# Optimization experiments

Hardware: AMD Instinct MI355X
Metric: run time of the kernel (lower is better)

## Reference

```python
import jax, jax.numpy as jnp
import numpy as np

H, B, N, D, VD, FFH = 8, 16, 512, 512, 64, 2048
NPICK = N // 2
NORM = 1.0 / np.sqrt(VD)


def _ha_encoder(h, W_query, W_key, W_val, W1, W2, W3, W4, W5, W6):
    # h: [B, N, D]; weights: [H, D, VD]
    np_ = NPICK
    pick, dlv = h[:, :np_], h[:, np_:]
    proj = lambda x, W: jnp.einsum('bnd,hdk->hbnk', x, W)
    Q, K, V = proj(h, W_query), proj(h, W_key), proj(h, W_val)
    Kp, Kd = K[:, :, :np_], K[:, :, np_:]   # shared projections (same W_key)
    Vp, Vd = V[:, :, :np_], V[:, :, np_:]
    Qp = proj(pick, W1); Qpap = proj(pick, W2); Qpad = proj(pick, W3)
    Qd = proj(dlv, W4);  Qdad = proj(dlv, W5);  Qdap = proj(dlv, W6)
    c_main = NORM * jnp.einsum('hbnk,hbmk->hbnm', Q, K)          # [H,B,N,N]
    c_pd = NORM * jnp.sum(Qp * Kd, -1)                           # [H,B,np] paired pick->delivery
    c_pap = NORM * jnp.einsum('hbnk,hbmk->hbnm', Qpap, Kp)       # pick -> all pick
    c_pad = NORM * jnp.einsum('hbnk,hbmk->hbnm', Qpad, Kd)       # pick -> all delivery
    c_dp = NORM * jnp.sum(Qd * Kp, -1)                           # paired delivery->pick
    c_dad = NORM * jnp.einsum('hbnk,hbmk->hbnm', Qdad, Kd)       # delivery -> all delivery
    c_dap = NORM * jnp.einsum('hbnk,hbmk->hbnm', Qdap, Kp)       # delivery -> all pick
    ninf1 = jnp.full((H, h.shape[0], np_), -jnp.inf, c_main.dtype)
    ninf2 = jnp.full((H, h.shape[0], np_, np_), -jnp.inf, c_main.dtype)
    col_pd = jnp.concatenate([c_pd, ninf1], 2)[..., None]        # [H,B,N,1]
    blk_pap = jnp.concatenate([c_pap, ninf2], 2)                 # [H,B,N,np]
    blk_pad = jnp.concatenate([c_pad, ninf2], 2)
    col_dp = jnp.concatenate([ninf1, c_dp], 2)[..., None]
    blk_dad = jnp.concatenate([ninf2, c_dad], 2)
    blk_dap = jnp.concatenate([ninf2, c_dap], 2)
    compat = jnp.concatenate([c_main, col_pd, blk_pap, blk_pad, col_dp, blk_dad, blk_dap], -1)
    a = jax.nn.softmax(compat, -1)                               # [H,B,N,N+2+4*np]
    zpad = jnp.zeros_like(Vd)
    V_add_d = jnp.concatenate([Vd, zpad], 2)                     # [H,B,N,VD]
    V_add_p = jnp.concatenate([zpad, Vp], 2)
    av = lambda w, v: jnp.einsum('hbnm,hbmv->hbnv', w, v)
    i = N
    heads = av(a[..., :N], V)
    heads = heads + a[..., i:i + 1] * V_add_d; i += 1
    heads = heads + av(a[..., i:i + np_], Vp); i += np_
    heads = heads + av(a[..., i:i + np_], Vd); i += np_
    heads = heads + a[..., i:i + 1] * V_add_p; i += 1
    heads = heads + av(a[..., i:i + np_], Vd); i += np_
    heads = heads + av(a[..., i:i + np_], Vp)
    return heads.transpose(1, 2, 0, 3).reshape(h.shape[0], N, H * VD)


def _split_heads(x):
    b, n, hd = x.shape
    return x.reshape(b, n, H, hd // H).transpose(0, 2, 1, 3)


def _mha(q, k, v):
    dk = q.shape[-1]
    w = jax.nn.softmax(jnp.einsum('bhnd,bhmd->bhnm', q, k) / np.sqrt(dk), -1)
    o = jnp.einsum('bhnm,bhmd->bhnd', w, v)
    b, hh, n, d = o.shape
    return o.transpose(0, 2, 1, 3).reshape(b, n, hh * d)


def _ff(x, w1, b1, w2, b2, a):
    return x + (jax.nn.relu(x @ w1 + b1) @ w2 + b2) * a


def _forward(x, W_query, W_key, W_val, W1_query, W2_query, W3_query, W4_query, W5_query, W6_query,
             Wq_w, Wk_w, Wv_w, Wq2p_w, Wq2d_w, Wk2_w, Wv2_w,
             comb_w, comb_b, comb2_w, comb2_b, comb3_w, comb3_b,
             alpha1, alpha2, alpha3,
             ff1_w1, ff1_b1, ff1_w2, ff1_b2, ffa1,
             ff2_w1, ff2_b1, ff2_w2, ff2_b2, ffa2,
             ff3_w1, ff3_b1, ff3_w2, ff3_b2, ffa3):
    # stage 1: heterogeneous attention block (combine_3 / AN3 / FF3)
    ha = _ha_encoder(x, W_query, W_key, W_val, W1_query, W2_query, W3_query, W4_query, W5_query, W6_query)
    out = x + (ha @ comb3_w + comb3_b) * alpha3
    out = _ff(out, ff3_w1, ff3_b1, ff3_w2, ff3_b2, ffa3)
    # stage 2: standard multi-head self-attention (combine / AN1 / FF1)
    q = _split_heads(out @ Wq_w); k = _split_heads(out @ Wk_w); v = _split_heads(out @ Wv_w)
    out = out + (_mha(q, k, v) @ comb_w + comb_b) * alpha1
    out = _ff(out, ff1_w1, ff1_b1, ff1_w2, ff1_b2, ffa1)
    # stage 3: pickup/delivery specific queries (combine_2 / AN2 / FF2)
    q2 = jnp.concatenate([out[:, :NPICK] @ Wq2p_w, out[:, NPICK:] @ Wq2d_w], 1)
    q2 = _split_heads(q2); k2 = _split_heads(out @ Wk2_w); v2 = _split_heads(out @ Wv2_w)
    out = out + (_mha(q2, k2, v2) @ comb2_w + comb2_b) * alpha2
    out = _ff(out, ff2_w1, ff2_b1, ff2_w2, ff2_b2, ffa2)
    return out


def setup_inputs() -> dict:
    key = jax.random.key(0)
    ks = jax.random.split(key, 64)
    it = iter(range(64))
    def nrm(shape):
        return jax.random.normal(ks[next(it)], shape, jnp.float32)
    def uni(shape):
        s = 1.0 / np.sqrt(shape[-1])  # torch init_parameters: uniform(-1/sqrt(size(-1)), ...)
        return jax.random.uniform(ks[next(it)], shape, jnp.float32, -s, s)
    d = {'x': nrm((B, N, D))}
    for n in ['W_query', 'W_key', 'W_val', 'W1_query', 'W2_query', 'W3_query', 'W4_query', 'W5_query', 'W6_query']:
        d[n] = uni((H, D, VD))
    for n in ['Wq_w', 'Wk_w', 'Wv_w', 'Wq2p_w', 'Wq2d_w', 'Wk2_w', 'Wv2_w']:
        d[n] = uni((D, H * VD))
    for n in ['comb_w', 'comb2_w', 'comb3_w']:
        d[n] = uni((H * VD, D))
    for n in ['comb_b', 'comb2_b', 'comb3_b']:
        d[n] = uni((D,))
    for n in ['alpha1', 'alpha2', 'alpha3']:
        d[n] = uni((1,))
    for i in ['1', '2', '3']:
        d['ff' + i + '_w1'] = uni((D, FFH))
        d['ff' + i + '_b1'] = uni((FFH,))
        d['ff' + i + '_w2'] = uni((FFH, D))
        d['ff' + i + '_b2'] = uni((D,))
        d['ffa' + i] = uni((1,))
    return d


def reference(x, W_query, W_key, W_val, W1_query, W2_query, W3_query, W4_query, W5_query, W6_query,
              Wq_w, Wk_w, Wv_w, Wq2p_w, Wq2d_w, Wk2_w, Wv2_w,
              comb_w, comb_b, comb2_w, comb2_b, comb3_w, comb3_b,
              alpha1, alpha2, alpha3,
              ff1_w1, ff1_b1, ff1_w2, ff1_b2, ffa1,
              ff2_w1, ff2_b1, ff2_w2, ff2_b2, ffa2,
              ff3_w1, ff3_b1, ff3_w2, ff3_b2, ffa3):
    return _forward(x, W_query, W_key, W_val, W1_query, W2_query, W3_query, W4_query, W5_query, W6_query,
                    Wq_w, Wk_w, Wv_w, Wq2p_w, Wq2d_w, Wk2_w, Wv2_w,
                    comb_w, comb_b, comb2_w, comb2_b, comb3_w, comb3_b,
                    alpha1, alpha2, alpha3,
                    ff1_w1, ff1_b1, ff1_w2, ff1_b2, ffa1,
                    ff2_w1, ff2_b1, ff2_w2, ff2_b2, ffa2,
                    ff3_w1, ff3_b1, ff3_w2, ff3_b2, ffa3)
```

## Files before the change

kernel.cpp:

```cpp
#include <hip/hip_runtime.h>
#include <math.h>

#define Hh 8
#define Bb 16
#define Nn 512
#define Dd 512
#define VDd 64
#define NPICKk 256
#define NORMF 0.125f
#define SCL2 0.1803368801f

typedef unsigned short ushortT;
typedef __bf16 bf16x8 __attribute__((ext_vector_type(8)));
typedef float f32x4 __attribute__((ext_vector_type(4)));

struct PtrsB { const ushortT* p[12]; };
struct PtrsD { ushortT* p[6]; };
struct Ptrs9 { const float* p[9]; };
struct Ptrs10 { const float* p[10]; };
struct Ptrs6 { const float* p[6]; };

__device__ inline ushortT f2bf(float f) {
    __bf16 h = (__bf16)f;
    union { __bf16 h; ushortT u; } v; v.h = h;
    return v.u;
}
__device__ inline float bf2f(ushortT u) {
    union { unsigned int u; float f; } v; v.u = ((unsigned int)u) << 16;
    return v.f;
}
__device__ inline float exp2fast(float x) {
#if __has_builtin(__builtin_amdgcn_exp2f)
    return __builtin_amdgcn_exp2f(x);
#else
    return exp2f(x);
#endif
}
__device__ inline void gload16(const void* gptr, void* ldsptr) {
    auto g = reinterpret_cast<const __attribute__((address_space(1))) unsigned int*>(
        reinterpret_cast<uintptr_t>(gptr));
    auto l = reinterpret_cast<__attribute__((address_space(3))) unsigned int*>(
        reinterpret_cast<uintptr_t>(ldsptr));
    __builtin_amdgcn_global_load_lds(g, l, 16, 0, 0);
}

#define LIX(r, g) (((r) << 6) + ((((g) ^ ((r) & 7))) << 3))

__global__ __launch_bounds__(256) void castx(const float* __restrict__ in,
                                             ushortT* __restrict__ out) {
    int i = blockIdx.x * 256 + threadIdx.x;
    float4 v = *(const float4*)&in[(size_t)i * 4];
    ushort4 o; o.x = f2bf(v.x); o.y = f2bf(v.y); o.z = f2bf(v.z); o.w = f2bf(v.w);
    *(ushort4*)&out[(size_t)i * 4] = o;
}

__device__ inline void tbody(const float* __restrict__ in, ushortT* __restrict__ out,
                             int in_ld, int out_ld, int r0, int c0) {
    __shared__ float T[64][65];
    int tr = threadIdx.x >> 4, tc4 = (threadIdx.x & 15) * 4;
#pragma unroll
    for (int p = 0; p < 4; ++p) {
        float4 v = *(const float4*)&in[(size_t)(r0 + tr + p * 16) * in_ld + c0 + tc4];
        T[tr + p * 16][tc4 + 0] = v.x; T[tr + p * 16][tc4 + 1] = v.y;
        T[tr + p * 16][tc4 + 2] = v.z; T[tr + p * 16][tc4 + 3] = v.w;
    }
    __syncthreads();
#pragma unroll
    for (int p = 0; p < 4; ++p) {
        int orow = c0 + tr + p * 16;
        int ocol = r0 + tc4;
        ushort4 o;
        o.x = f2bf(T[tc4 + 0][tr + p * 16]);
        o.y = f2bf(T[tc4 + 1][tr + p * 16]);
        o.z = f2bf(T[tc4 + 2][tr + p * 16]);
        o.w = f2bf(T[tc4 + 3][tr + p * 16]);
        *(ushort4*)&out[(size_t)orow * out_ld + ocol] = o;
    }
}

__global__ __launch_bounds__(256) void thead(Ptrs9 s, ushortT* __restrict__ dst) {
    int w = blockIdx.z >> 3, h = blockIdx.z & 7;
    tbody(s.p[w] + (size_t)h * 512 * 64,
          dst + (size_t)w * 262144 + (size_t)h * 64 * 512,
          64, 512, blockIdx.y * 64, 0);
}
__global__ __launch_bounds__(256) void tsq(Ptrs10 s, ushortT* __restrict__ dst) {
    tbody(s.p[blockIdx.z], dst + (size_t)blockIdx.z * 262144,
          512, 512, blockIdx.y * 64, blockIdx.x * 64);
}
__global__ __launch_bounds__(256) void tff(Ptrs6 s, ushortT* __restrict__ dst) {
    int z = blockIdx.z;
    if (z < 3) { if (blockIdx.y >= 8 || blockIdx.x >= 32) return; }
    else       { if (blockIdx.y >= 32 || blockIdx.x >= 8) return; }
    int in_ld = (z < 3) ? 2048 : 512;
    int out_ld = (z < 3) ? 512 : 2048;
    tbody(s.p[z], dst + (size_t)z * 1048576, in_ld, out_ld,
          blockIdx.y * 64, blockIdx.x * 64);
}

__global__ __launch_bounds__(256) void gemm_bf(
    PtrsB Bp, PtrsD Db, const ushortT* __restrict__ A, float* __restrict__ outF,
    int M, int N, int K, const float* __restrict__ bias,
    const float* __restrict__ res, const float* __restrict__ alpha,
    int do_relu, int nroute, int vtmask, int scmask)
{
    __shared__ __align__(16) ushortT As[128 * 64];
    __shared__ __align__(16) ushortT Bs[128 * 64];
    const int tid = threadIdx.x;
    const int wid = tid >> 6, lane = tid & 63;
    const int wm = wid >> 1, wn = wid & 1;
    const int l15 = lane & 15, l4 = lane >> 4;

    int bid = blockIdx.y * gridDim.x + blockIdx.x;
    int nwg = gridDim.x * gridDim.y;
    int q = nwg >> 3;
    int swz = (bid & 7) * q + (bid >> 3);
    int bx = swz % gridDim.x, by = swz / gridDim.x;

    const int r0 = by * 128, c0 = bx * 128;
    const int half = ((r0 & (Nn - 1)) >= NPICKk) ? 1 : 0;
    const ushortT* Bt = Bp.p[((c0 >> 9) << 1) | half];
    const int cB = nroute ? (c0 & 511) : c0;

    const ushortT* aSrc[4];
    const ushortT* bSrc[4];
    char* ldsA[4];
    char* ldsB[4];
#pragma unroll
    for (int i = 0; i < 4; ++i) {
        int off = wid * 4096 + i * 1024 + lane * 16;
        int row = off >> 7;
        int sg = ((off >> 4) & 7) ^ (row & 7);
        aSrc[i] = A + (size_t)(r0 + row) * K + sg * 8;
        bSrc[i] = Bt + (size_t)(cB + row) * K + sg * 8;
        ldsA[i] = (char*)As + off;
        ldsB[i] = (char*)Bs + off;
    }

    f32x4 acc[4][4] = {};

    for (int kt = 0; kt < K; kt += 64) {
        __syncthreads();
#pragma unroll
        for (int i = 0; i < 4; ++i) {
            gload16(aSrc[i] + kt, ldsA[i]);
            gload16(bSrc[i] + kt, ldsB[i]);
        }
        asm volatile("s_waitcnt vmcnt(0)" ::: "memory");
        __syncthreads();
#pragma unroll
        for (int kk = 0; kk < 2; ++kk) {
            int g0 = kk * 4 + l4;
            bf16x8 af[4], bfv[4];
#pragma unroll
            for (int mi = 0; mi < 4; ++mi)
                af[mi] = *(const bf16x8*)&As[LIX(wm * 64 + mi * 16 + l15, g0)];
#pragma unroll
            for (int ni = 0; ni < 4; ++ni)
                bfv[ni] = *(const bf16x8*)&Bs[LIX(wn * 64 + ni * 16 + l15, g0)];
#pragma unroll
            for (int mi = 0; mi < 4; ++mi)
#pragma unroll
                for (int ni = 0; ni < 4; ++ni)
                    acc[mi][ni] = __builtin_amdgcn_mfma_f32_16x16x32_bf16(
                        bfv[ni], af[mi], acc[mi][ni], 0, 0, 0);
        }
    }

    if (nroute) {
#pragma unroll
        for (int mi = 0; mi < 4; ++mi) {
            int row = r0 + wm * 64 + mi * 16 + l15;
#pragma unroll
            for (int ni = 0; ni < 4; ++ni) {
                int col = c0 + wn * 64 + ni * 16 + l4 * 4;
                int range = col >> 9, cc = col & 511;
                ushortT* d = Db.p[range];
                f32x4 a = acc[mi][ni];
                if ((scmask >> range) & 1) {
                    a[0] *= SCL2; a[1] *= SCL2; a[2] *= SCL2; a[3] *= SCL2;
                }
                if ((vtmask >> range) & 1) {
                    size_t vb = ((size_t)(row >> 9) * Hh + (cc >> 6)) * 64 + (cc & 63);
                    int tok = row & 511;
#pragma unroll
                    for (int r = 0; r < 4; ++r)
                        d[((vb + r) << 9) + tok] = f2bf(a[r]);
                } else {
                    ushort4 o;
                    o.x = f2bf(a[0]); o.y = f2bf(a[1]);
                    o.z = f2bf(a[2]); o.w = f2bf(a[3]);
                    *(ushort4*)&d[((size_t)row << 9) + cc] = o;
                }
            }
        }
    } else {
        const float alp = alpha ? alpha[0] : 1.0f;
        ushortT* outB = Db.p[0];
#pragma unroll
        for (int mi = 0; mi < 4; ++mi) {
            int row = r0 + wm * 64 + mi * 16 + l15;
#pragma unroll
            for (int ni = 0; ni < 4; ++ni) {
                int colb = c0 + wn * 64 + ni * 16 + l4 * 4;
                f32x4 a = acc[mi][ni];
                if (bias) {
                    float4 b4 = *(const float4*)&bias[colb];
                    a[0] += b4.x; a[1] += b4.y; a[2] += b4.z; a[3] += b4.w;
                }
                if (do_relu) {
#pragma unroll
                    for (int r = 0; r < 4; ++r) a[r] = fmaxf(a[r], 0.f);
                }
#pragma unroll
                for (int r = 0; r < 4; ++r) a[r] *= alp;
                size_t idx = (size_t)row * N + colb;
                if (res) {
                    float4 r4 = *(const float4*)&res[idx];
                    a[0] += r4.x; a[1] += r4.y; a[2] += r4.z; a[3] += r4.w;
                }
                if (outF)
                    *(float4*)&outF[idx] = make_float4(a[0], a[1], a[2], a[3]);
                if (outB) {
                    ushort4 o;
                    o.x = f2bf(a[0]); o.y = f2bf(a[1]);
                    o.z = f2bf(a[2]); o.w = f2bf(a[3]);
                    *(ushort4*)&outB[idx] = o;
                }
            }
        }
    }
}

__global__ __launch_bounds__(256) void gemm64(
    const ushortT* __restrict__ Bw, const ushortT* __restrict__ A,
    float* __restrict__ outF, ushortT* __restrict__ outB,
    int M, int N, int K, const float* __restrict__ bias,
    const float* __restrict__ resf, const ushortT* __restrict__ resb,
    const float* __restrict__ alpha, int do_relu)
{
    __shared__ __align__(16) ushortT As[64 * 64];
    __shared__ __align__(16) ushortT Bs[128 * 64];
    const int tid = threadIdx.x;
    const int wid = tid >> 6, lane = tid & 63;
    const int wm = wid >> 1, wn = wid & 1;
    const int l15 = lane & 15, l4 = lane >> 4;

    int bid = blockIdx.y * gridDim.x + blockIdx.x;
    int nwg = gridDim.x * gridDim.y;
    int q = nwg >> 3;
    int swz = (bid & 7) * q + (bid >> 3);
    int bx = swz % gridDim.x, by = swz / gridDim.x;
    const int r0 = by * 64, c0 = bx * 128;

    const ushortT* aSrc[2];
    char* ldsA[2];
#pragma unroll
    for (int i = 0; i < 2; ++i) {
        int off = wid * 2048 + i * 1024 + lane * 16;
        int row = off >> 7;
        int sg = ((off >> 4) & 7) ^ (row & 7);
        aSrc[i] = A + (size_t)(r0 + row) * K + sg * 8;
        ldsA[i] = (char*)As + off;
    }
    const ushortT* bSrc[4];
    char* ldsB[4];
#pragma unroll
    for (int i = 0; i < 4; ++i) {
        int off = wid * 4096 + i * 1024 + lane * 16;
        int row = off >> 7;
        int sg = ((off >> 4) & 7) ^ (row & 7);
        bSrc[i] = Bw + (size_t)(c0 + row) * K + sg * 8;
        ldsB[i] = (char*)Bs + off;
    }

    f32x4 acc[2][4] = {};

    for (int kt = 0; kt < K; kt += 64) {
        __syncthreads();
#pragma unroll
        for (int i = 0; i < 2; ++i) gload16(aSrc[i] + kt, ldsA[i]);
#pragma unroll
        for (int i = 0; i < 4; ++i) gload16(bSrc[i] + kt, ldsB[i]);
        asm volatile("s_waitcnt vmcnt(0)" ::: "memory");
        __syncthreads();
#pragma unroll
        for (int kk = 0; kk < 2; ++kk) {
            int g0 = kk * 4 + l4;
            bf16x8 af[2], bfv[4];
#pragma unroll
            for (int mi = 0; mi < 2; ++mi)
                af[mi] = *(const bf16x8*)&As[LIX(wm * 32 + mi * 16 + l15, g0)];
#pragma unroll
            for (int ni = 0; ni < 4; ++ni)
                bfv[ni] = *(const bf16x8*)&Bs[LIX(wn * 64 + ni * 16 + l15, g0)];
#pragma unroll
            for (int mi = 0; mi < 2; ++mi)
#pragma unroll
                for (int ni = 0; ni < 4; ++ni)
                    acc[mi][ni] = __builtin_amdgcn_mfma_f32_16x16x32_bf16(
                        bfv[ni], af[mi], acc[mi][ni], 0, 0, 0);
        }
    }

    const float alp = alpha ? alpha[0] : 1.0f;
#pragma unroll
    for (int mi = 0; mi < 2; ++mi) {
        int row = r0 + wm * 32 + mi * 16 + l15;
#pragma unroll
        for (int ni = 0; ni < 4; ++ni) {
            int colb = c0 + wn * 64 + ni * 16 + l4 * 4;
            f32x4 a = acc[mi][ni];
            if (bias) {
                float4 b4 = *(const float4*)&bias[colb];
                a[0] += b4.x; a[1] += b4.y; a[2] += b4.z; a[3] += b4.w;
            }
            if (do_relu) {
#pragma unroll
                for (int r = 0; r < 4; ++r) a[r] = fmaxf(a[r], 0.f);
            }
#pragma unroll
            for (int r = 0; r < 4; ++r) a[r] *= alp;
            size_t idx = (size_t)row * N + colb;
            if (resf) {
                float4 r4 = *(const float4*)&resf[idx];
                a[0] += r4.x; a[1] += r4.y; a[2] += r4.z; a[3] += r4.w;
            }
            if (resb) {
                ushort4 r4 = *(const ushort4*)&resb[idx];
                a[0] += bf2f(r4.x); a[1] += bf2f(r4.y);
                a[2] += bf2f(r4.z); a[3] += bf2f(r4.w);
            }
            if (outF)
                *(float4*)&outF[idx] = make_float4(a[0], a[1], a[2], a[3]);
            if (outB) {
                ushort4 o;
                o.x = f2bf(a[0]); o.y = f2bf(a[1]);
                o.z = f2bf(a[2]); o.w = f2bf(a[3]);
                *(ushort4*)&outB[idx] = o;
            }
        }
    }
}

__global__ __launch_bounds__(256) void diag_dot_bb(const ushortT* __restrict__ QD,
                                                   const ushortT* __restrict__ K,
                                                   float* __restrict__ Sdg) {
    int i = blockIdx.x * 256 + threadIdx.x;
    int h = i & 7, n = (i >> 3) & 511, b = i >> 12;
    int dix = (n < NPICKk) ? n + NPICKk : n - NPICKk;
    const ushortT* q = QD + (((size_t)(b * Nn + n) * Hh + h) << 6);
    const ushortT* k = K + (((size_t)(b * Nn + dix) * Hh + h) << 6);
    float s = 0.f;
#pragma unroll
    for (int d = 0; d < 64; d += 4) {
        ushort4 a = *(const ushort4*)(q + d);
        ushort4 c = *(const ushort4*)(k + d);
        s += bf2f(a.x) * bf2f(c.x) + bf2f(a.y) * bf2f(c.y)
           + bf2f(a.z) * bf2f(c.z) + bf2f(a.w) * bf2f(c.w);
    }
    Sdg[i] = s;
}

template <int HA>
__global__ __launch_bounds__(256) void attn10(
    const ushortT* __restrict__ Qm, const ushortT* __restrict__ Km,
    const ushortT* __restrict__ Vtm, const ushortT* __restrict__ QAm,
    const ushortT* __restrict__ QBm, const float* __restrict__ Sdg,
    ushortT* __restrict__ Out)
{
    __shared__ __align__(16) ushortT Ks[64 * 64];
    __shared__ __align__(16) ushortT Vs[64 * 64];
    __shared__ __align__(16) ushortT Pw[4][16 * 64];
    __shared__ float sdl[64];

    const int tid = threadIdx.x, wid = tid >> 6, lane = tid & 63;
    const int l15 = lane & 15, l4 = lane >> 4;

    const int p = blockIdx.x + (blockIdx.y << 3) + (blockIdx.z << 6);
    const int n0 = (((p >> 3) & 7)) << 6;
    const int g8 = (p & 7) | ((p >> 6) << 3);
    const int h = g8 & 7, b = g8 >> 3;
    const int bh = b * Hh + h;

    const size_t qrow = (((size_t)(b * Nn + n0 + wid * 16 + l15) * Hh + h) << 6);
    bf16x8 qf[2], xaf[2], xbf[2];
#pragma unroll
    for (int kk = 0; kk < 2; ++kk) {
        int g0 = kk * 4 + l4;
        qf[kk] = *(const bf16x8*)&Qm[qrow + g0 * 8];
        if (HA) {
            xaf[kk] = *(const bf16x8*)&QAm[qrow + g0 * 8];
            xbf[kk] = *(const bf16x8*)&QBm[qrow + g0 * 8];
        }
    }
    if (HA && tid < 64) sdl[tid] = Sdg[((size_t)(b * Nn + n0 + tid)) * Hh + h];
    const int td = (n0 < NPICKk) ? ((n0 + NPICKk) >> 6) : ((n0 - NPICKk) >> 6);

    const ushortT* kSrc[2]; ushortT* kDst[2];
    const ushortT* vSrc[2]; ushortT* vDst[2];
#pragma unroll
    for (int i = 0; i < 2; ++i) {
        int off = wid * 2048 + i * 1024 + lane * 16;
        int row = off >> 7, sg = ((off >> 4) & 7) ^ (row & 7);
        kSrc[i] = Km + (((size_t)(b * Nn + row) * Hh + h) << 6) + sg * 8;
        kDst[i] = (ushortT*)((char*)Ks + off);
        vSrc[i] = Vtm + (((size_t)(bh * 64 + row)) << 9) + sg * 8;
        vDst[i] = (ushortT*)((char*)Vs + off);
    }

    float M[4], Lp[4];
    f32x4 Oa[4] = {};
#pragma unroll
    for (int r = 0; r < 4; ++r) { M[r] = -INFINITY; Lp[r] = 0.f; }

    bf16x8 krbuf[2][2], vrbuf[2][2];
#pragma unroll
    for (int i = 0; i < 2; ++i) {
        krbuf[0][i] = *(const bf16x8*)kSrc[i];
        vrbuf[0][i] = *(const bf16x8*)vSrc[i];
    }

#pragma unroll
    for (int t = 0; t < 8; ++t) {
        const int cur = t & 1, nxt = cur ^ 1;
        __builtin_amdgcn_s_barrier();
#pragma unroll
        for (int i = 0; i < 2; ++i) {
            *(bf16x8*)kDst[i] = krbuf[cur][i];
            *(bf16x8*)vDst[i] = vrbuf[cur][i];
        }
        if (t < 7) {
#pragma unroll
            for (int i = 0; i < 2; ++i) {
                krbuf[nxt][i] = *(const bf16x8*)(kSrc[i] + (size_t)(t + 1) * (64 * Hh * VDd));
                vrbuf[nxt][i] = *(const bf16x8*)(vSrc[i] + (t + 1) * 64);
            }
        }
        asm volatile("s_waitcnt lgkmcnt(0)" ::: "memory");
        __builtin_amdgcn_s_barrier();
        __builtin_amdgcn_sched_barrier(0);

        __builtin_amdgcn_s_setprio(1);
        f32x4 s1[4] = {}, sX[4] = {};
#pragma unroll
        for (int kk = 0; kk < 2; ++kk) {
            bf16x8 aq = qf[kk];
            bf16x8 ax;
            if (HA) ax = (t >= 4) ? xbf[kk] : xaf[kk];
#pragma unroll
            for (int ni = 0; ni < 4; ++ni) {
                bf16x8 bk = *(const bf16x8*)&Ks[LIX(ni * 16 + l15, kk * 4 + l4)];
                s1[ni] = __builtin_amdgcn_mfma_f32_16x16x32_bf16(aq, bk, s1[ni], 0, 0, 0);
                if (HA)
                    sX[ni] = __builtin_amdgcn_mfma_f32_16x16x32_bf16(ax, bk, sX[ni], 0, 0, 0);
            }
        }
        __builtin_amdgcn_s_setprio(0);

        const bool dt = HA && (t == td);

        float mloc[4];
        bool grow = false;
#pragma unroll
        for (int r = 0; r < 4; ++r) {
            int rw = wid * 16 + l4 * 4 + r;
            float m = s1[0][r];
#pragma unroll
            for (int ni = 1; ni < 4; ++ni) m = fmaxf(m, s1[ni][r]);
            if (HA) {
#pragma unroll
                for (int ni = 0; ni < 4; ++ni) m = fmaxf(m, sX[ni][r]);
            }
            if (dt && l15 == l4 * 4 + r) m = fmaxf(m, sdl[rw]);
            mloc[r] = m;
            grow = grow || (m > M[r] + 8.f);
        }
        if (__any(grow)) {
#pragma unroll
            for (int r = 0; r < 4; ++r) {
                float m = mloc[r];
#pragma unroll
                for (int o = 8; o >= 1; o >>= 1) m = fmaxf(m, __shfl_xor(m, o, 16));
                float mn = fmaxf(M[r], m);
                float sc = exp2fast(M[r] - mn);
                M[r] = mn; Lp[r] *= sc;
#pragma unroll
                for (int ni = 0; ni < 4; ++ni) Oa[ni][r] *= sc;
            }
        }

#pragma unroll
        for (int r = 0; r < 4; ++r) {
            int rw = wid * 16 + l4 * 4 + r;
            float rs = 0.f;
#pragma unroll
            for (int ni = 0; ni < 4; ++ni) {
                float pv = exp2fast(s1[ni][r] - M[r]);
                if (HA) pv += exp2fast(sX[ni][r] - M[r]);
                if (dt && ni == wid && l15 == l4 * 4 + r) pv += exp2fast(sdl[rw] - M[r]);
                s1[ni][r] = pv;
                rs += pv;
            }
            Lp[r] += rs;
        }

#pragma unroll
        for (int ni = 0; ni < 4; ++ni)
#pragma unroll
            for (int r = 0; r < 4; ++r) {
                int prow = l4 * 4 + r;
                int col = ni * 16 + l15;
                Pw[wid][(prow << 6) + ((((col >> 3) ^ (prow & 7))) << 3) + (col & 7)] =
                    f2bf(s1[ni][r]);
            }

        __builtin_amdgcn_s_setprio(1);
#pragma unroll
        for (int kk = 0; kk < 2; ++kk) {
            int g0 = kk * 4 + l4;
            bf16x8 ap = *(const bf16x8*)&Pw[wid][LIX(l15, g0)];
#pragma unroll
            for (int ni = 0; ni < 4; ++ni) {
                bf16x8 bv = *(const bf16x8*)&Vs[LIX(ni * 16 + l15, g0)];
                Oa[ni] = __builtin_amdgcn_mfma_f32_16x16x32_bf16(ap, bv, Oa[ni], 0, 0, 0);
            }
        }
        __builtin_amdgcn_s_setprio(0);
    }

#pragma unroll
    for (int r = 0; r < 4; ++r) {
        float l = Lp[r];
#pragma unroll
        for (int o = 8; o >= 1; o >>= 1) l += __shfl_xor(l, o, 16);
        float inv = 1.0f / l;
        size_t obase = (((size_t)(b * Nn + n0 + wid * 16 + l4 * 4 + r) * Hh + h) << 6);
#pragma unroll
        for (int ni = 0; ni < 4; ++ni)
            Out[obase + ni * 16 + l15] = f2bf(Oa[ni][r] * inv);
    }
}

extern "C" void kernel_launch(void* const* d_in, const int* in_sizes, int n_in,
                              void* d_out, int out_size, void* d_ws, size_t ws_size,
                              hipStream_t stream)
{
    const float* x = (const float*)d_in[0];

    int dictOrder = (in_sizes[18] != 512);
    const float* comb_w  = (const float*)d_in[17];
    const float* comb2_w = (const float*)d_in[dictOrder ? 18 : 19];
    const float* comb3_w = (const float*)d_in[dictOrder ? 19 : 21];
    const float* comb_b  = (const float*)d_in[dictOrder ? 20 : 18];
    const float* comb2_b = (const float*)d_in[dictOrder ? 21 : 20];
    const float* comb3_b = (const float*)d_in[22];
    const float* alpha1 = (const float*)d_in[23];
    const float* alpha2 = (const float*)d_in[24];
    const float* alpha3 = (const float*)d_in[25];
    const float* ff1_w1 = (const float*)d_in[26];
    const float* ff1_b1 = (const float*)d_in[27];
    const float* ff1_w2 = (const float*)d_in[28];
    const float* ff1_b2 = (const float*)d_in[29];
    const float* ffa1   = (const float*)d_in[30];
    const float* ff2_w1 = (const float*)d_in[31];
    const float* ff2_b1 = (const float*)d_in[32];
    const float* ff2_w2 = (const float*)d_in[33];
    const float* ff2_b2 = (const float*)d_in[34];
    const float* ffa2   = (const float*)d_in[35];
    const float* ff3_w1 = (const float*)d_in[36];
    const float* ff3_b1 = (const float*)d_in[37];
    const float* ff3_w2 = (const float*)d_in[38];
    const float* ff3_b2 = (const float*)d_in[39];
    const float* ffa3   = (const float*)d_in[40];

    char* W = (char*)d_ws;
    ushortT* wbHead = (ushortT*)(W + 0);
    ushortT* wbMha  = (ushortT*)(W + 4718592);
    ushortT* wbComb = (ushortT*)(W + 8388608);
    ushortT* wbFf1  = (ushortT*)(W + 9961472);
    ushortT* wbFf2  = (ushortT*)(W + 16252928);
    ushortT* xbf    = (ushortT*)(W + 22544384);
    float*   Sd     = (float*)  (W + 30932992);
    ushortT* bufQ   = (ushortT*)(W + 31195136);
    ushortT* bufK   = (ushortT*)(W + 39583744);
    ushortT* bufVt  = (ushortT*)(W + 47972352);
    ushortT* bufQA  = (ushortT*)(W + 56360960);
    ushortT* bufQB  = (ushortT*)(W + 64749568);
    ushortT* bufQD  = (ushortT*)(W + 73138176);
    ushortT* hidden = (ushortT*)(W + 81526784);
    ushortT* curb   = (ushortT*)(W + 115081216);
    ushortT* bufHA  = xbf;
    float*   cur    = (float*)d_out;

    dim3 tb(256);
    const int TOK = Bb * Nn;
    const size_t WS = 512 * 512;
    const size_t WF = 2048 * 512;

    hipLaunchKernelGGL(castx, dim3(TOK * 512 / 1024), tb, 0, stream, x, xbf);
    {
        Ptrs9 s; for (int i = 0; i < 9; ++i) s.p[i] = (const float*)d_in[1 + i];
        hipLaunchKernelGGL(thead, dim3(1, 8, 72), tb, 0, stream, s, wbHead);
    }
    {
        Ptrs10 s;
        for (int i = 0; i < 7; ++i) s.p[i] = (const float*)d_in[10 + i];
        s.p[7] = comb_w; s.p[8] = comb2_w; s.p[9] = comb3_w;
        hipLaunchKernelGGL(tsq, dim3(8, 8, 10), tb, 0, stream, s, wbMha);
    }
    {
        Ptrs6 s;
        s.p[0] = ff1_w1; s.p[1] = ff2_w1; s.p[2] = ff3_w1;
        s.p[3] = ff1_w2; s.p[4] = ff2_w2; s.p[5] = ff3_w2;
        hipLaunchKernelGGL(tff, dim3(32, 32, 6), tb, 0, stream, s, wbFf1);
    }

    auto gemm = [&](PtrsB Bp, PtrsD Db, const ushortT* A, float* oF,
                    int M, int Ncc, int Kc, const float* bias, const float* res,
                    const float* alp, int relu, int nroute, int vtmask, int scmask) {
        hipLaunchKernelGGL(gemm_bf, dim3(Ncc / 128, M / 128), tb, 0, stream,
                           Bp, Db, A, oF, M, Ncc, Kc, bias, res, alp, relu, nroute,
                           vtmask, scmask);
    };
    auto g64 = [&](const ushortT* Bw, const ushortT* A, float* oF, ushortT* oB,
                   int M, int Ncc, int Kc, const float* bias, const float* resf,
                   const ushortT* resb, const float* alp, int relu) {
        hipLaunchKernelGGL(gemm64, dim3(Ncc / 128, M / 64), tb, 0, stream,
                           Bw, A, oF, oB, M, Ncc, Kc, bias, resf, resb, alp, relu);
    };
    auto uni = [&](const ushortT* w) { PtrsB b; for (int i = 0; i < 12; ++i) b.p[i] = w; return b; };
    auto d1 = [&](ushortT* d) { PtrsD dd = {}; dd.p[0] = d; return dd; };

    {
        PtrsB b;
        b.p[0] = b.p[1] = wbHead + 0 * WS;
        b.p[2] = b.p[3] = wbHead + 1 * WS;
        b.p[4] = b.p[5] = wbHead + 2 * WS;
        b.p[6] = wbHead + 4 * WS; b.p[7] = wbHead + 8 * WS;
        b.p[8] = wbHead + 5 * WS; b.p[9] = wbHead + 7 * WS;
        b.p[10] = wbHead + 3 * WS; b.p[11] = wbHead + 6 * WS;
        PtrsD d; d.p[0] = bufQ; d.p[1] = bufK; d.p[2] = bufVt;
        d.p[3] = bufQA; d.p[4] = bufQB; d.p[5] = bufQD;
        gemm(b, d, xbf, nullptr, TOK, 3072, 512, nullptr, nullptr, nullptr, 0, 6, 4, 57);
    }

    hipLaunchKernelGGL(diag_dot_bb, dim3(Bb * Nn * Hh / 256), tb, 0, stream, bufQD, bufK, Sd);
    hipLaunchKernelGGL((attn10<1>), dim3(Nn / 64, Hh, Bb), tb, 0, stream,
                       bufQ, bufK, bufVt, bufQA, bufQB, Sd, bufHA);

    g64(wbComb + 2 * WS, bufHA, nullptr, curb, TOK, 512, 512, comb3_b, x, nullptr, alpha3, 0);
    gemm(uni(wbFf1 + 2 * WF), d1(hidden), curb, nullptr, TOK, 2048, 512, ff3_b1, nullptr, nullptr, 1, 0, 0, 0);
    g64(wbFf2 + 2 * WF, hidden, nullptr, curb, TOK, 512, 2048, ff3_b2, nullptr, curb, ffa3, 0);

    {
        PtrsB b;
        b.p[0] = b.p[1] = wbMha + 0 * WS;
        b.p[2] = b.p[3] = wbMha + 1 * WS;
        b.p[4] = b.p[5] = wbMha + 2 * WS;
        PtrsD d = {}; d.p[0] = bufQ; d.p[1] = bufK; d.p[2] = bufVt;
        gemm(b, d, curb, nullptr, TOK, 1536, 512, nullptr, nullptr, nullptr, 0, 3, 4, 1);
    }
    hipLaunchKernelGGL((attn10<0>), dim3(Nn / 64, Hh, Bb), tb, 0, stream,
                       bufQ, bufK, bufVt, nullptr, nullptr, nullptr, bufHA);
    g64(wbComb + 0 * WS, bufHA, nullptr, curb, TOK, 512, 512, comb_b, nullptr, curb, alpha1, 0);
    gemm(uni(wbFf1 + 0 * WF), d1(hidden), curb, nullptr, TOK, 2048, 512, ff1_b1, nullptr, nullptr, 1, 0, 0, 0);
    g64(wbFf2 + 0 * WF, hidden, nullptr, curb, TOK, 512, 2048, ff1_b2, nullptr, curb, ffa1, 0);

    {
        PtrsB b;
        b.p[0] = wbMha + 3 * WS; b.p[1] = wbMha + 4 * WS;
        b.p[2] = b.p[3] = wbMha + 5 * WS;
        b.p[4] = b.p[5] = wbMha + 6 * WS;
        PtrsD d = {}; d.p[0] = bufQ; d.p[1] = bufK; d.p[2] = bufVt;
        gemm(b, d, curb, nullptr, TOK, 1536, 512, nullptr, nullptr, nullptr, 0, 3, 4, 1);
    }
    hipLaunchKernelGGL((attn10<0>), dim3(Nn / 64, Hh, Bb), tb, 0, stream,
                       bufQ, bufK, bufVt, nullptr, nullptr, nullptr, bufHA);
    g64(wbComb + 1 * WS, bufHA, nullptr, curb, TOK, 512, 512, comb2_b, nullptr, curb, alpha2, 0);
    gemm(uni(wbFf1 + 1 * WF), d1(hidden), curb, nullptr, TOK, 2048, 512, ff2_b1, nullptr, nullptr, 1, 0, 0, 0);
    g64(wbFf2 + 1 * WF, hidden, cur, nullptr, TOK, 512, 2048, ff2_b2, nullptr, curb, ffa2, 0);
}
```

Before: 474.9 us.

## Double-buffer LDS tiles in bf16 GEMM with two-stage prefetch

The GEMM kernel now keeps two LDS buffers for the A and B tiles and prefetches the tile two k-steps ahead. Partial vmcnt waits let global-to-LDS loads overlap the MFMA compute instead of stalling on every tile. This doubles shared memory use to 64KB per block, which can lower occupancy. It also relies on hand-placed barriers and waitcnt values being correct.

New measurement: 460.6 us. 1.03x faster.

```diff
diff --git a/kernel.cpp b/kernel.cpp
--- a/kernel.cpp
+++ b/kernel.cpp
@@ -104,8 +104,8 @@
     const float* __restrict__ res, const float* __restrict__ alpha,
     int do_relu, int nroute, int vtmask, int scmask)
 {
-    __shared__ __align__(16) ushortT As[128 * 64];
-    __shared__ __align__(16) ushortT Bs[128 * 64];
+    __shared__ __align__(16) ushortT As[2][128 * 64];
+    __shared__ __align__(16) ushortT Bs[2][128 * 64];
     const int tid = threadIdx.x;
     const int wid = tid >> 6, lane = tid & 63;
     const int wm = wid >> 1, wn = wid & 1;
@@ -124,8 +124,7 @@
 
     const ushortT* aSrc[4];
     const ushortT* bSrc[4];
-    char* ldsA[4];
-    char* ldsB[4];
+    int offv[4];
 #pragma unroll
     for (int i = 0; i < 4; ++i) {
         int off = wid * 4096 + i * 1024 + lane * 16;
@@ -133,37 +132,57 @@
         int sg = ((off >> 4) & 7) ^ (row & 7);
         aSrc[i] = A + (size_t)(r0 + row) * K + sg * 8;
         bSrc[i] = Bt + (size_t)(cB + row) * K + sg * 8;
-        ldsA[i] = (char*)As + off;
-        ldsB[i] = (char*)Bs + off;
+        offv[i] = off;
+    }
+
+    const int nkt = K >> 6;
+#pragma unroll
+    for (int i = 0; i < 4; ++i) {
+        gload16(aSrc[i], (char*)As[0] + offv[i]);
+        gload16(bSrc[i], (char*)Bs[0] + offv[i]);
+    }
+#pragma unroll
+    for (int i = 0; i < 4; ++i) {
+        gload16(aSrc[i] + 64, (char*)As[1] + offv[i]);
+        gload16(bSrc[i] + 64, (char*)Bs[1] + offv[i]);
     }
 
     f32x4 acc[4][4] = {};
 
-    for (int kt = 0; kt < K; kt += 64) {
-        __syncthreads();
-#pragma unroll
-        for (int i = 0; i < 4; ++i) {
-            gload16(aSrc[i] + kt, ldsA[i]);
-            gload16(bSrc[i] + kt, ldsB[i]);
-        }
-        asm volatile("s_waitcnt vmcnt(0)" ::: "memory");
-        __syncthreads();
+    for (int t = 0; t < nkt; ++t) {
+        const int cur = t & 1;
+        if (t == nkt - 1) asm volatile("s_waitcnt vmcnt(0)" ::: "memory");
+        else              asm volatile("s_waitcnt vmcnt(8)" ::: "memory");
+        __builtin_amdgcn_s_barrier();
+        __builtin_amdgcn_sched_barrier(0);
+        const ushortT* Ac = As[cur];
+        const ushortT* Bc = Bs[cur];
 #pragma unroll
         for (int kk = 0; kk < 2; ++kk) {
             int g0 = kk * 4 + l4;
             bf16x8 af[4], bfv[4];
 #pragma unroll
             for (int mi = 0; mi < 4; ++mi)
-                af[mi] = *(const bf16x8*)&As[LIX(wm * 64 + mi * 16 + l15, g0)];
+                af[mi] = *(const bf16x8*)&Ac[LIX(wm * 64 + mi * 16 + l15, g0)];
 #pragma unroll
             for (int ni = 0; ni < 4; ++ni)
-                bfv[ni] = *(const bf16x8*)&Bs[LIX(wn * 64 + ni * 16 + l15, g0)];
+                bfv[ni] = *(const bf16x8*)&Bc[LIX(wn * 64 + ni * 16 + l15, g0)];
 #pragma unroll
             for (int mi = 0; mi < 4; ++mi)
 #pragma unroll
                 for (int ni = 0; ni < 4; ++ni)
                     acc[mi][ni] = __builtin_amdgcn_mfma_f32_16x16x32_bf16(
                         bfv[ni], af[mi], acc[mi][ni], 0, 0, 0);
+        }
+        __builtin_amdgcn_s_barrier();
+        asm volatile("" ::: "memory");
+        if (t + 2 < nkt) {
+            int kt2 = (t + 2) << 6;
+#pragma unroll
+            for (int i = 0; i < 4; ++i) {
+                gload16(aSrc[i] + kt2, (char*)As[cur] + offv[i]);
+                gload16(bSrc[i] + kt2, (char*)Bs[cur] + offv[i]);
+            }
         }
     }
 
```
